# Optimization experiments

Measured on AMD Instinct MI355X. Metric: run time of the kernel, lower is better.

The kernel has to match this reference:

```python
import jax, jax.numpy as jnp
import numpy as np

D_MODEL = 2048
NUM_HEADS = 16
NUM_GROUPS = 4
HEAD_DIM = D_MODEL // NUM_HEADS  # 128; note d_model//num_groups == num_groups*head_dim


def setup_inputs() -> dict:
    key = jax.random.key(0)
    ks = jax.random.split(key, 11)
    B, S, D = 4, 1024, D_MODEL
    dk = D // NUM_GROUPS  # 512
    s = 0.02
    return {
        "query": jax.random.normal(ks[0], (B, S, D), jnp.float32),
        "key": jax.random.normal(ks[1], (B, S, D), jnp.float32),
        "value": jax.random.normal(ks[2], (B, S, D), jnp.float32),
        "Wq": jax.random.normal(ks[3], (D, D), jnp.float32) * s,
        "bq": jnp.zeros((D,), jnp.float32),
        "Wk": jax.random.normal(ks[4], (D, dk), jnp.float32) * s,
        "bk": jnp.zeros((dk,), jnp.float32),
        "Wv": jax.random.normal(ks[5], (D, dk), jnp.float32) * s,
        "bv": jnp.zeros((dk,), jnp.float32),
        "Wo": jax.random.normal(ks[6], (D, D), jnp.float32) * s,
        "bo": jnp.zeros((D,), jnp.float32),
    }


def reference(query, key, value, Wq, bq, Wk, bk, Wv, bv, Wo, bo):
    B, S, D = query.shape
    rep = NUM_HEADS // NUM_GROUPS
    # projections
    q = query @ Wq + bq                      # [B,S,D]
    k = key @ Wk + bk                        # [B,S,D//G]
    v = value @ Wv + bv                      # [B,S,D//G]
    # split heads: q -> [B,H,S,hd]; k,v -> [B,G,S,hd] (valid since D//G == G*hd)
    q = q.reshape(B, S, NUM_HEADS, HEAD_DIM).transpose(0, 2, 1, 3)
    k = k.reshape(B, S, NUM_GROUPS, HEAD_DIM).transpose(0, 2, 1, 3)
    v = v.reshape(B, S, NUM_GROUPS, HEAD_DIM).transpose(0, 2, 1, 3)
    # repeat_interleave KV groups to match heads: [B,H,S,hd]
    k = jnp.repeat(k, rep, axis=1)
    v = jnp.repeat(v, rep, axis=1)
    scale = 1.0 / jnp.sqrt(jnp.float32(HEAD_DIM))
    scores = jnp.einsum("bhqd,bhkd->bhqk", q, k) * scale  # [B,H,S,S]
    attn_weights = jax.nn.softmax(scores, axis=-1)
    attn_output = jnp.einsum("bhqk,bhkd->bhqd", attn_weights, v)
    attn_output = attn_output.transpose(0, 2, 1, 3).reshape(B, S, D)
    output = attn_output @ Wo + bo
    return output, attn_weights
```

## Files before the change

kernel.cpp:

```cpp
#include <hip/hip_runtime.h>
#include <hip/hip_bf16.h>

typedef unsigned short u16;
typedef __attribute__((ext_vector_type(8))) short short8;
typedef __attribute__((ext_vector_type(4))) float f32x4;

__device__ __forceinline__ u16 f2bf(float f) {
  __hip_bfloat16 h = __float2bfloat16(f);
  return *reinterpret_cast<u16*>(&h);
}

struct TP4 {
  const float *s0, *s1, *s2, *s3;
  u16 *d0, *d1, *d2, *d3;
};
__global__ __launch_bounds__(256)
void transpose4_kernel(TP4 tp) {
  const int z = blockIdx.z;
  const float* sf; u16* dst; int C;
  if      (z == 0) { sf = tp.s0; dst = tp.d0; C = 2048; }
  else if (z == 1) { sf = tp.s1; dst = tp.d1; C = 512;  }
  else if (z == 2) { sf = tp.s2; dst = tp.d2; C = 512;  }
  else             { sf = tp.s3; dst = tp.d3; C = 2048; }
  const int c0 = blockIdx.x * 32, r0 = blockIdx.y * 32;
  if (c0 >= C) return;
  const int R = 2048;
  __shared__ u16 tile[32][33];
  const int tx = threadIdx.x, ty = threadIdx.y;
#pragma unroll
  for (int i = 0; i < 4; ++i) {
    int r = r0 + ty + i * 8;
    tile[ty + i * 8][tx] = f2bf(sf[(long)r * C + c0 + tx]);
  }
  __syncthreads();
#pragma unroll
  for (int i = 0; i < 4; ++i) {
    int rr = ty + i * 8;
    dst[(long)(c0 + rr) * R + r0 + tx] = tile[tx][rr];
  }
}

#define BM 128
#define BN 128
#define BK 64

struct GemmP {
  const void* A;
  const u16* B;
  const float* bias;
  void* C;
  int N, K, lda, ldb, ldc, mode;
  float scale;
};
struct Gemm3 {
  GemmP q[3];
  int nb0, nb1;
  int nwg;
};

template<bool AF32>
__global__ __launch_bounds__(256, 2)
void gemm3_kernel(Gemm3 g) {
  __shared__ __align__(16) u16 lds[2][2][BM * BK];
  const int t = threadIdx.x;
  const int w = t >> 6, l = t & 63;

  const int cpx = g.nwg >> 3;
  const int swz = (blockIdx.x & 7) * cpx + (blockIdx.x >> 3);
  int pi, local;
  if (swz < g.nb0)            { pi = 0; local = swz; }
  else if (swz < g.nb0 + g.nb1) { pi = 1; local = swz - g.nb0; }
  else                        { pi = 2; local = swz - g.nb0 - g.nb1; }
  const GemmP p = g.q[pi];

  const int nTn = p.N / BN;
  const int tm = (local / nTn) * BM;
  const int tn = (local % nTn) * BN;

  const u16*   Ab = (const u16*)p.A + (long)tm * p.lda;
  const float* Af = (const float*)p.A + (long)tm * p.lda;
  const u16*   Bt = p.B + (long)tn * p.ldb;

  const int wr = w >> 1, wc = w & 1;
  f32x4 acc[4][4] = {};
  float aR[32];

  auto stageB = [&](int kt, int buf) {
#pragma unroll
    for (int i = 0; i < 4; ++i) {
      int c = i * 256 + t;
      int row = c >> 3;
      int slot = (c & 7) ^ (row & 7);
      const u16* gp = Bt + kt * BK + (long)row * p.ldb + slot * 8;
      u16* lp = &lds[buf][1][(i * 256 + w * 64) * 8];
      __builtin_amdgcn_global_load_lds(
          (const __attribute__((address_space(1))) unsigned int*)gp,
          (__attribute__((address_space(3))) unsigned int*)lp, 16, 0, 0);
    }
  };
  auto stageA_bf16 = [&](int kt, int buf) {
#pragma unroll
    for (int i = 0; i < 4; ++i) {
      int c = i * 256 + t;
      int row = c >> 3;
      int slot = (c & 7) ^ (row & 7);
      const u16* gp = Ab + kt * BK + (long)row * p.lda + slot * 8;
      u16* lp = &lds[buf][0][(i * 256 + w * 64) * 8];
      __builtin_amdgcn_global_load_lds(
          (const __attribute__((address_space(1))) unsigned int*)gp,
          (__attribute__((address_space(3))) unsigned int*)lp, 16, 0, 0);
    }
  };
  auto loadA_f32 = [&](int kt) {
    const float* g0 = Af + kt * BK;
#pragma unroll
    for (int i = 0; i < 4; ++i) {
      int c = i * 256 + t;
      int row = c >> 3, slot = c & 7;
      const float4* gp = (const float4*)(g0 + (long)row * p.lda + slot * 8);
      float4 v0 = gp[0], v1 = gp[1];
      aR[i * 8 + 0] = v0.x; aR[i * 8 + 1] = v0.y; aR[i * 8 + 2] = v0.z; aR[i * 8 + 3] = v0.w;
      aR[i * 8 + 4] = v1.x; aR[i * 8 + 5] = v1.y; aR[i * 8 + 6] = v1.z; aR[i * 8 + 7] = v1.w;
    }
  };
  auto writeA = [&](int buf) {
#pragma unroll
    for (int i = 0; i < 4; ++i) {
      int c = i * 256 + t;
      int row = c >> 3, slot = c & 7;
      short8 o;
#pragma unroll
      for (int j = 0; j < 8; ++j) o[j] = (short)f2bf(aR[i * 8 + j]);
      *(short8*)&lds[buf][0][row * 64 + ((slot ^ (row & 7)) * 8)] = o;
    }
  };
  auto compute = [&](int buf) {
    const u16* At  = lds[buf][0];
    const u16* Btl = lds[buf][1];
#pragma unroll
    for (int ks = 0; ks < 2; ++ks) {
      short8 af[4], bfr[4];
#pragma unroll
      for (int mi = 0; mi < 4; ++mi) {
        int row = wr * 64 + mi * 16 + (l & 15);
        int slot = (ks * 4 + (l >> 4)) ^ (row & 7);
        af[mi] = *(const short8*)&At[row * 64 + slot * 8];
      }
#pragma unroll
      for (int ni = 0; ni < 4; ++ni) {
        int row = wc * 64 + ni * 16 + (l & 15);
        int slot = (ks * 4 + (l >> 4)) ^ (row & 7);
        bfr[ni] = *(const short8*)&Btl[row * 64 + slot * 8];
      }
#pragma unroll
      for (int mi = 0; mi < 4; ++mi)
#pragma unroll
        for (int ni = 0; ni < 4; ++ni)
          acc[mi][ni] = __builtin_amdgcn_mfma_f32_16x16x32_bf16(
              af[mi], bfr[ni], acc[mi][ni], 0, 0, 0);
    }
  };

  const int nkt = p.K / BK;
  if (AF32) { loadA_f32(0); stageB(0, 0); writeA(0); }
  else      { stageA_bf16(0, 0); stageB(0, 0); }
  __syncthreads();

  int buf = 0;
  for (int kt = 0; kt < nkt; ++kt) {
    if (kt + 1 < nkt) {
      if (AF32) loadA_f32(kt + 1); else stageA_bf16(kt + 1, buf ^ 1);
      stageB(kt + 1, buf ^ 1);
    }
    compute(buf);
    if (AF32 && kt + 1 < nkt) writeA(buf ^ 1);
    __syncthreads();
    buf ^= 1;
  }

  const int cl = l & 15, rj = (l >> 4) * 4;
#pragma unroll
  for (int mi = 0; mi < 4; ++mi) {
#pragma unroll
    for (int ni = 0; ni < 4; ++ni) {
      int cidx = tn + wc * 64 + ni * 16 + cl;
      float bv = p.bias ? p.bias[cidx] : 0.f;
#pragma unroll
      for (int j = 0; j < 4; ++j) {
        int r = tm + wr * 64 + mi * 16 + rj + j;
        float v = acc[mi][ni][j] * p.scale + bv;
        if (p.mode == 2) {
          ((u16*)p.C)[((long)(r >> 10)) * 524288 + (long)cidx * 1024 + (r & 1023)] = f2bf(v);
        } else {
          long idx = (long)r * p.ldc + cidx;
          if (p.mode == 1) ((u16*)p.C)[idx] = f2bf(v);
          else             ((float*)p.C)[idx] = v;
        }
      }
    }
  }
}

__global__ __launch_bounds__(512, 4)
void fused_attn_kernel(const u16* __restrict__ Qg, const u16* __restrict__ Kg,
                       const u16* __restrict__ Vg, float* __restrict__ attnF,
                       u16* __restrict__ AO) {
  __shared__ __align__(16) u16 kv[2][2][64 * 128];
  __shared__ __align__(16) u16 p4[2][2][32 * 64];
  float* red = (float*)&p4[1][0][0];

  const int t = threadIdx.x;
  const int w = t >> 6, l = t & 63;
  const int wq = w >> 2, wcol = w & 3;
  const int qb = blockIdx.x, z = blockIdx.y;
  const int b = z >> 4, h = z & 15, g = h >> 2;
  const int q0 = qb * 32;
  const int qi = wq * 16 + (l & 15);

  const u16* Qbase = Qg + ((long)b * 1024 + q0) * 2048 + h * 128;
  const u16* Kbase = Kg + (long)b * 1024 * 512 + g * 128;
  const u16* Vbase = Vg + ((long)b * 512 + g * 128) * 1024;
  float* attnO = attnF + ((long)z * 1024 + q0) * 1024;

  auto glds16 = [](const u16* gp, u16* lp) {
    __builtin_amdgcn_global_load_lds(
        (const __attribute__((address_space(1))) unsigned int*)gp,
        (__attribute__((address_space(3))) unsigned int*)lp, 16, 0, 0);
  };
  auto stageK = [&](int c, int pb, int sub) {
#pragma unroll
    for (int i = 0; i < 2; ++i) {
      int idx = i * 512 + t;
      int row = idx >> 4, blk = idx & 15;
      glds16(Kbase + (long)(c * 64 + row) * 512 + ((blk ^ (row & 7)) * 8),
             &kv[pb][sub][(i * 512 + w * 64) * 8]);
    }
  };
  auto stageV = [&](int c, int pb, int sub) {
#pragma unroll
    for (int i = 0; i < 2; ++i) {
      int idx = i * 512 + t;
      int row = idx >> 3, blk = idx & 7;
      glds16(Vbase + (long)row * 1024 + c * 64 + ((blk ^ (row & 7)) * 8),
             &kv[pb][sub][(i * 512 + w * 64) * 8]);
    }
  };

  {
    int row = t >> 4, blk = t & 15;
    glds16(Qbase + (long)row * 2048 + ((blk ^ (row & 7)) * 8), &((u16*)p4)[(w * 64) * 8]);
  }
  stageK(0, 0, 0);
  stageK(1, 0, 1);
  __syncthreads();

  short8 qf[4];
  {
    const u16* pq = (const u16*)p4;
#pragma unroll
    for (int ks = 0; ks < 4; ++ks) {
      int slot = (ks * 4 + (l >> 4)) ^ (qi & 7);
      qf[ks] = *(const short8*)&pq[qi * 128 + slot * 8];
    }
  }

  f32x4 acc[16];
#pragma unroll
  for (int c = 0; c < 16; ++c) acc[c] = (f32x4){0.f, 0.f, 0.f, 0.f};

  const int krow = wcol * 16 + (l & 15);
#pragma unroll
  for (int pph = 0; pph < 8; ++pph) {
    if (pph < 7) {
      stageK(2 * pph + 2, (pph + 1) & 1, 0);
      stageK(2 * pph + 3, (pph + 1) & 1, 1);
    } else {
      stageV(0, 0, 0);
      stageV(1, 0, 1);
    }
    __builtin_amdgcn_s_setprio(1);
#pragma unroll
    for (int sub = 0; sub < 2; ++sub) {
      const int c = 2 * pph + sub;
      const u16* Kl = kv[pph & 1][sub];
#pragma unroll
      for (int ks = 0; ks < 4; ++ks) {
        int slot = (ks * 4 + (l >> 4)) ^ (krow & 7);
        short8 kf = *(const short8*)&Kl[krow * 128 + slot * 8];
        acc[c] = __builtin_amdgcn_mfma_f32_16x16x32_bf16(kf, qf[ks], acc[c], 0, 0, 0);
      }
    }
    __builtin_amdgcn_s_setprio(0);
    __syncthreads();
  }

  const float scale = 0.08838834764831845f;
  float jm[4] = {-1e30f, -1e30f, -1e30f, -1e30f};
#pragma unroll
  for (int c = 0; c < 16; ++c) {
#pragma unroll
    for (int j = 0; j < 4; ++j) jm[j] = fmaxf(jm[j], acc[c][j]);
  }
  float mx = fmaxf(fmaxf(jm[0], jm[1]), fmaxf(jm[2], jm[3]));
  mx = fmaxf(mx, __shfl_xor(mx, 16));
  mx = fmaxf(mx, __shfl_xor(mx, 32));
  if ((l >> 4) == 0) red[wcol * 32 + qi] = mx;
  __syncthreads();
  const float m = fmaxf(fmaxf(red[0 * 32 + qi], red[1 * 32 + qi]),
                        fmaxf(red[2 * 32 + qi], red[3 * 32 + qi]));
  __syncthreads();
  float s4[4] = {0.f, 0.f, 0.f, 0.f};
#pragma unroll
  for (int c = 0; c < 16; ++c) {
#pragma unroll
    for (int j = 0; j < 4; ++j) {
      float e = __expf((acc[c][j] - m) * scale);
      acc[c][j] = e;
      s4[j] += e;
    }
  }
  float ss = (s4[0] + s4[1]) + (s4[2] + s4[3]);
  ss += __shfl_xor(ss, 16);
  ss += __shfl_xor(ss, 32);
  if ((l >> 4) == 0) red[wcol * 32 + qi] = ss;
  __syncthreads();
  const float inv = 1.0f / (red[0 * 32 + qi] + red[1 * 32 + qi] +
                            red[2 * 32 + qi] + red[3 * 32 + qi]);

#pragma unroll
  for (int c = 0; c < 16; ++c) acc[c] = acc[c] * inv;

  const int kloc = wcol * 16 + ((l >> 4) * 4);
  auto pwrite = [&](u16* dst, const f32x4& a) {
    int blk = (kloc >> 3) ^ (qi & 7);
    uint2 val;
    val.x = (unsigned)f2bf(a[0]) | ((unsigned)f2bf(a[1]) << 16);
    val.y = (unsigned)f2bf(a[2]) | ((unsigned)f2bf(a[3]) << 16);
    *(uint2*)&dst[qi * 64 + blk * 8 + (kloc & 7)] = val;
  };

  pwrite(p4[0][0], acc[0]);
  pwrite(p4[0][1], acc[1]);
  __syncthreads();

  f32x4 acc2[2] = {};
  const int prow = wq * 16 + (l & 15);
#pragma unroll
  for (int pp = 0; pp < 8; ++pp) {
    if (pp < 7) {
      pwrite(p4[(pp + 1) & 1][0], acc[2 * pp + 2]);
      pwrite(p4[(pp + 1) & 1][1], acc[2 * pp + 3]);
      stageV(2 * pp + 2, (pp + 1) & 1, 0);
      stageV(2 * pp + 3, (pp + 1) & 1, 1);
    }
    __builtin_amdgcn_s_setprio(1);
#pragma unroll
    for (int sub = 0; sub < 2; ++sub) {
      const u16* Vl = kv[pp & 1][sub];
      const u16* Pl = p4[pp & 1][sub];
#pragma unroll
      for (int ks = 0; ks < 2; ++ks) {
        int ablk = (ks * 4 + (l >> 4)) ^ (prow & 7);
        short8 af = *(const short8*)&Pl[prow * 64 + ablk * 8];
#pragma unroll
        for (int ni = 0; ni < 2; ++ni) {
          int vrow = wcol * 32 + ni * 16 + (l & 15);
          int vslot = (ks * 4 + (l >> 4)) ^ (vrow & 7);
          short8 vf = *(const short8*)&Vl[vrow * 64 + vslot * 8];
          acc2[ni] = __builtin_amdgcn_mfma_f32_16x16x32_bf16(af, vf, acc2[ni], 0, 0, 0);
        }
      }
    }
    __builtin_amdgcn_s_setprio(0);
    __syncthreads();
  }

#pragma unroll
  for (int c = 0; c < 16; ++c)
    *(f32x4*)(attnO + (long)qi * 1024 + c * 64 + wcol * 16 + ((l >> 4) * 4)) = acc[c];

  u16* AObase = AO + ((long)b * 1024 + q0) * 2048 + h * 128;
#pragma unroll
  for (int ni = 0; ni < 2; ++ni)
#pragma unroll
    for (int j = 0; j < 4; ++j) {
      int qq = wq * 16 + (l >> 4) * 4 + j;
      int d = wcol * 32 + ni * 16 + (l & 15);
      AObase[(long)qq * 2048 + d] = f2bf(acc2[ni][j]);
    }
}

extern "C" void kernel_launch(void* const* d_in, const int* in_sizes, int n_in,
                              void* d_out, int out_size, void* d_ws, size_t ws_size,
                              hipStream_t stream) {
  const float* query = (const float*)d_in[0];
  const float* key_  = (const float*)d_in[1];
  const float* value = (const float*)d_in[2];
  const float* Wq = (const float*)d_in[3]; const float* bq = (const float*)d_in[4];
  const float* Wk = (const float*)d_in[5]; const float* bk = (const float*)d_in[6];
  const float* Wv = (const float*)d_in[7]; const float* bv = (const float*)d_in[8];
  const float* Wo = (const float*)d_in[9]; const float* bo = (const float*)d_in[10];

  float* outF  = (float*)d_out;
  float* attnF = outF + 8388608;

  char* wp = (char*)d_ws;
  u16* WqT = (u16*)wp; wp += 2048L * 2048 * 2;
  u16* WkT = (u16*)wp; wp += 512L * 2048 * 2;
  u16* WvT = (u16*)wp; wp += 512L * 2048 * 2;
  u16* WoT = (u16*)wp; wp += 2048L * 2048 * 2;
  u16* Qb  = (u16*)wp; wp += 4096L * 2048 * 2;
  u16* Kb  = (u16*)wp; wp += 4096L * 512 * 2;
  u16* VT  = (u16*)wp; wp += 4L * 512 * 1024 * 2;
  u16* AO  = (u16*)wp; wp += 4096L * 2048 * 2;

  TP4 tp;
  tp.s0 = Wq; tp.s1 = Wk; tp.s2 = Wv; tp.s3 = Wo;
  tp.d0 = WqT; tp.d1 = WkT; tp.d2 = WvT; tp.d3 = WoT;
  transpose4_kernel<<<dim3(64, 64, 4), dim3(32, 8), 0, stream>>>(tp);

  Gemm3 g = {};
  g.q[0].A = query; g.q[0].B = WqT; g.q[0].bias = bq; g.q[0].C = Qb;
  g.q[0].N = 2048; g.q[0].K = 2048; g.q[0].lda = 2048; g.q[0].ldb = 2048;
  g.q[0].ldc = 2048; g.q[0].mode = 1; g.q[0].scale = 1.f;
  g.q[1].A = key_; g.q[1].B = WkT; g.q[1].bias = bk; g.q[1].C = Kb;
  g.q[1].N = 512; g.q[1].K = 2048; g.q[1].lda = 2048; g.q[1].ldb = 2048;
  g.q[1].ldc = 512; g.q[1].mode = 1; g.q[1].scale = 1.f;
  g.q[2].A = value; g.q[2].B = WvT; g.q[2].bias = bv; g.q[2].C = VT;
  g.q[2].N = 512; g.q[2].K = 2048; g.q[2].lda = 2048; g.q[2].ldb = 2048;
  g.q[2].ldc = 1024; g.q[2].mode = 2; g.q[2].scale = 1.f;
  g.nb0 = 512; g.nb1 = 128; g.nwg = 768;
  gemm3_kernel<true><<<dim3(768), 256, 0, stream>>>(g);

  fused_attn_kernel<<<dim3(32, 64), 512, 0, stream>>>(Qb, Kb, VT, attnF, AO);

  Gemm3 go = {};
  go.q[0].A = AO; go.q[0].B = WoT; go.q[0].bias = bo; go.q[0].C = outF;
  go.q[0].N = 2048; go.q[0].K = 2048; go.q[0].lda = 2048; go.q[0].ldb = 2048;
  go.q[0].ldc = 2048; go.q[0].mode = 0; go.q[0].scale = 1.f;
  go.nb0 = 512; go.nb1 = 0; go.nwg = 512;
  gemm3_kernel<false><<<dim3(512), 256, 0, stream>>>(go);
}
```

Before: 295.5 us.

## Stage K chunks through a four-slot ring with three chunks in flight

Replaces the paired double-buffered K staging with a 4-slot LDS ring. Three 64-row K chunks stay in flight, gated by explicit vmcnt waits and raw s_barrier per chunk instead of a full __syncthreads per pair. The aim is deeper prefetch of K during the QK^T MFMA loop, to hide global-load latency. The cost is twice as many barriers and reliance on hand-counted outstanding loads for correctness, including the V prefetch placed into slots 0/1.

After: 295.9 us. About the same (+0.1%).

```diff
diff --git a/kernel.cpp b/kernel.cpp
--- a/kernel.cpp
+++ b/kernel.cpp
@@ -208,6 +208,7 @@
   __shared__ __align__(16) u16 kv[2][2][64 * 128];
   __shared__ __align__(16) u16 p4[2][2][32 * 64];
   float* red = (float*)&p4[1][0][0];
+  u16* kvf = &kv[0][0][0];
 
   const int t = threadIdx.x;
   const int w = t >> 6, l = t & 63;
@@ -227,32 +228,36 @@
         (const __attribute__((address_space(1))) unsigned int*)gp,
         (__attribute__((address_space(3))) unsigned int*)lp, 16, 0, 0);
   };
-  auto stageK = [&](int c, int pb, int sub) {
+  auto stageKf = [&](int c, int buf) {
 #pragma unroll
     for (int i = 0; i < 2; ++i) {
       int idx = i * 512 + t;
       int row = idx >> 4, blk = idx & 15;
       glds16(Kbase + (long)(c * 64 + row) * 512 + ((blk ^ (row & 7)) * 8),
-             &kv[pb][sub][(i * 512 + w * 64) * 8]);
-    }
-  };
-  auto stageV = [&](int c, int pb, int sub) {
+             &kvf[buf * 8192 + (i * 512 + w * 64) * 8]);
+    }
+  };
+  auto stageVf = [&](int c, int buf) {
 #pragma unroll
     for (int i = 0; i < 2; ++i) {
       int idx = i * 512 + t;
       int row = idx >> 3, blk = idx & 7;
       glds16(Vbase + (long)row * 1024 + c * 64 + ((blk ^ (row & 7)) * 8),
-             &kv[pb][sub][(i * 512 + w * 64) * 8]);
-    }
-  };
+             &kvf[buf * 8192 + (i * 512 + w * 64) * 8]);
+    }
+  };
+  auto stageV = [&](int c, int pb, int sub) { stageVf(c, pb * 2 + sub); };
 
   {
     int row = t >> 4, blk = t & 15;
     glds16(Qbase + (long)row * 2048 + ((blk ^ (row & 7)) * 8), &((u16*)p4)[(w * 64) * 8]);
   }
-  stageK(0, 0, 0);
-  stageK(1, 0, 1);
-  __syncthreads();
+  stageKf(0, 0);
+  stageKf(1, 1);
+  stageKf(2, 2);
+  asm volatile("s_waitcnt vmcnt(4)" ::: "memory");
+  __builtin_amdgcn_sched_barrier(0);
+  __builtin_amdgcn_s_barrier();
 
   short8 qf[4];
   {
@@ -270,28 +275,24 @@
 
   const int krow = wcol * 16 + (l & 15);
 #pragma unroll
-  for (int pph = 0; pph < 8; ++pph) {
-    if (pph < 7) {
-      stageK(2 * pph + 2, (pph + 1) & 1, 0);
-      stageK(2 * pph + 3, (pph + 1) & 1, 1);
-    } else {
-      stageV(0, 0, 0);
-      stageV(1, 0, 1);
-    }
+  for (int c = 0; c < 16; ++c) {
+    const u16* Kl = &kvf[(c & 3) * 8192];
     __builtin_amdgcn_s_setprio(1);
 #pragma unroll
-    for (int sub = 0; sub < 2; ++sub) {
-      const int c = 2 * pph + sub;
-      const u16* Kl = kv[pph & 1][sub];
-#pragma unroll
-      for (int ks = 0; ks < 4; ++ks) {
-        int slot = (ks * 4 + (l >> 4)) ^ (krow & 7);
-        short8 kf = *(const short8*)&Kl[krow * 128 + slot * 8];
-        acc[c] = __builtin_amdgcn_mfma_f32_16x16x32_bf16(kf, qf[ks], acc[c], 0, 0, 0);
-      }
+    for (int ks = 0; ks < 4; ++ks) {
+      int slot = (ks * 4 + (l >> 4)) ^ (krow & 7);
+      short8 kf = *(const short8*)&Kl[krow * 128 + slot * 8];
+      acc[c] = __builtin_amdgcn_mfma_f32_16x16x32_bf16(kf, qf[ks], acc[c], 0, 0, 0);
     }
     __builtin_amdgcn_s_setprio(0);
-    __syncthreads();
+    __builtin_amdgcn_s_barrier();
+    if (c + 3 < 16)      stageKf(c + 3, (c + 3) & 3);
+    else if (c + 3 < 18) stageVf(c + 3 - 16, (c + 3) & 3);
+    if (c < 15) {
+      asm volatile("s_waitcnt vmcnt(4)" ::: "memory");
+      __builtin_amdgcn_sched_barrier(0);
+      __builtin_amdgcn_s_barrier();
+    }
   }
 
   const float scale = 0.08838834764831845f;
```
